# Kernel tuning notes

Hardware: AMD Instinct MI355X
Metric: run time of the kernel (lower is better)

## Reference

```python
import jax, jax.numpy as jnp
import numpy as np

TOP_K = 2
CAPACITY_FACTOR = 1.0


def _ffn(x, w1, w2):
    # SwiGLU FFN: x [N, D], w1 [D, 2F], w2 [F, D]
    h = x @ w1
    x1, x2 = jnp.split(h, 2, axis=-1)
    return (x1 * jax.nn.silu(x2)) @ w2


def setup_inputs() -> dict:
    key = jax.random.key(0)
    ks = jax.random.split(key, 6)
    B, S, D, F, E_r, E_s = 4, 2048, 2048, 1024, 7, 1
    sc_in = 1.0 / np.sqrt(D)
    sc_mid = 1.0 / np.sqrt(F)
    return {
        "x": jax.random.normal(ks[0], (B, S, D), dtype=jnp.float32),
        "gate_w": jax.random.normal(ks[1], (D, E_r), dtype=jnp.float32) * sc_in,
        "expert_bias": jnp.zeros((E_r,), dtype=jnp.float32),
        "shared_w1": jax.random.normal(ks[2], (E_s, D, 2 * F), dtype=jnp.float32) * sc_in,
        "shared_w2": jax.random.normal(ks[3], (E_s, F, D), dtype=jnp.float32) * sc_mid,
        "routed_w1": jax.random.normal(ks[4], (E_r, D, 2 * F), dtype=jnp.float32) * sc_in,
        "routed_w2": jax.random.normal(ks[5], (E_r, F, D), dtype=jnp.float32) * sc_mid,
    }


def reference(x, gate_w, expert_bias, shared_w1, shared_w2, routed_w1, routed_w2):
    B, S, D = x.shape
    E_r = gate_w.shape[1]
    T = B * S
    capacity = max(1, int(CAPACITY_FACTOR * T / E_r))
    flat_x = x.reshape(T, D)

    # shared experts: applied to every token, summed
    shared_sum = jax.vmap(_ffn, in_axes=(None, 0, 0))(flat_x, shared_w1, shared_w2).sum(0)

    # gating (eval mode: no noise, no dropout)
    gate_logits = flat_x @ gate_w + expert_bias  # [T, E_r]
    aff = jax.nn.sigmoid(gate_logits)
    _, topk_idx = jax.lax.top_k(aff, TOP_K)  # [T, K]
    # mask[t, e] = expert e is among token t's top-k
    mask = (topk_idx[:, :, None] == jnp.arange(E_r)[None, None, :]).any(axis=1)  # [T, E_r]

    # per-expert capacity selection: keep top-`capacity` masked tokens by affinity
    score = jnp.where(mask, aff, -1.0).T  # [E_r, T]; aff >= 0 so -1 sorts last
    _, sel_idx = jax.lax.top_k(score, capacity)  # [E_r, capacity] token ids
    kept = jnp.take_along_axis(mask.T, sel_idx, axis=1)  # [E_r, cap]
    w = jnp.where(kept, jnp.take_along_axis(aff.T, sel_idx, axis=1), 0.0)  # [E_r, cap]

    # grouped gather -> FFN -> weighted scatter-add
    inp = flat_x[sel_idx]  # [E_r, cap, D]
    out = jax.vmap(_ffn)(inp, routed_w1, routed_w2)  # [E_r, cap, D]
    routed_sum = jnp.zeros_like(flat_x).at[sel_idx].add(out * w[:, :, None])

    return (shared_sum + routed_sum).reshape(B, S, D)
```

## Files before the change

kernel.cpp:

```cpp
#include <hip/hip_runtime.h>
#include <hip/hip_bf16.h>

typedef unsigned long long u64;
typedef __bf16 bf16x8 __attribute__((ext_vector_type(8)));
typedef float f32x4 __attribute__((ext_vector_type(4)));
typedef unsigned short ushort8_t __attribute__((ext_vector_type(8)));

#define TOKS 8192
#define DMODEL 2048
#define FD 1024
#define NEXP 7
#define CAP 1170
#define CAPP 1280
#define URT 134

#define MFMA16(a, b, c) __builtin_amdgcn_mfma_f32_16x16x32_bf16(a, b, c, 0, 0, 0)

__device__ __forceinline__ unsigned short f2bf(float f) {
  __hip_bfloat16 b = __float2bfloat16(f);
  return __builtin_bit_cast(unsigned short, b);
}
__device__ __forceinline__ float bf2f(unsigned short u) {
  __hip_bfloat16 b = __builtin_bit_cast(__hip_bfloat16, u);
  return __bfloat162float(b);
}
__device__ __forceinline__ void gload_lds16(const void* g, void* l) {
  __builtin_amdgcn_global_load_lds(
      (const __attribute__((address_space(1))) void*)g,
      (__attribute__((address_space(3))) void*)l, 16, 0, 0);
}

__global__ __launch_bounds__(256) void k_conv_gate(
    const float* __restrict__ x, const float* __restrict__ gw,
    const float* __restrict__ bias, unsigned short* __restrict__ xb,
    u64* __restrict__ keys) {
  const int t = blockIdx.x;
  const int tid = threadIdx.x;
  const int lane = tid & 63, wv = tid >> 6;
  const float* xr = x + (long)t * DMODEL;
  const int i0 = tid * 8;
  float4 v0 = *(const float4*)&xr[i0];
  float4 v1 = *(const float4*)&xr[i0 + 4];
  float xv[8] = {v0.x, v0.y, v0.z, v0.w, v1.x, v1.y, v1.z, v1.w};
  ushort8_t o;
#pragma unroll
  for (int j = 0; j < 8; ++j) o[j] = f2bf(xv[j]);
  *(ushort8_t*)&xb[(long)t * DMODEL + i0] = o;
  double acc[NEXP];
#pragma unroll
  for (int e = 0; e < NEXP; ++e) acc[e] = 0.0;
#pragma unroll
  for (int j = 0; j < 8; ++j) {
    const float* g = gw + (long)(i0 + j) * NEXP;
    double xd = (double)xv[j];
#pragma unroll
    for (int e = 0; e < NEXP; ++e) acc[e] += xd * (double)g[e];
  }
#pragma unroll
  for (int e = 0; e < NEXP; ++e)
    for (int off = 32; off > 0; off >>= 1)
      acc[e] += __shfl_down(acc[e], off, 64);
  __shared__ double red[4][NEXP];
  if (lane == 0)
#pragma unroll
    for (int e = 0; e < NEXP; ++e) red[wv][e] = acc[e];
  __syncthreads();
  if (tid == 0) {
    float aff[NEXP];
#pragma unroll
    for (int e = 0; e < NEXP; ++e) {
      double lg = red[0][e] + red[1][e] + red[2][e] + red[3][e] + (double)bias[e];
      aff[e] = (float)(1.0 / (1.0 + exp(-lg)));
    }
    int i1 = 0;
    for (int e = 1; e < NEXP; ++e) if (aff[e] > aff[i1]) i1 = e;
    int i2 = -1;
    for (int e = 0; e < NEXP; ++e) {
      if (e == i1) continue;
      if (i2 < 0 || aff[e] > aff[i2]) i2 = e;
    }
#pragma unroll
    for (int e = 0; e < NEXP; ++e) {
      u64 key = (u64)(0xFFFFFFFFu - (unsigned)t);
      if (e == i1 || e == i2) key |= ((u64)__float_as_uint(aff[e])) << 32;
      keys[(long)e * TOKS + t] = key;
    }
  }
}

template <bool PERM>
__global__ void k_transpose_bf16(const float* __restrict__ in0,
                                 const float* __restrict__ inr,
                                 unsigned short* __restrict__ out,
                                 int R, int C) {
  __shared__ float tile[32][33];
  int z = blockIdx.z;
  const float* in = (z == 0) ? in0 : (inr + (long)(z - 1) * R * C);
  unsigned short* o = out + (long)z * R * C;
  int c0 = blockIdx.x * 32;
  int r0 = blockIdx.y * 32;
  int tx = threadIdx.x, ty = threadIdx.y;
#pragma unroll
  for (int k = 0; k < 4; ++k)
    tile[ty + 8 * k][tx] = in[(long)(r0 + ty + 8 * k) * C + c0 + tx];
  __syncthreads();
#pragma unroll
  for (int k = 0; k < 4; ++k) {
    int c = c0 + ty + 8 * k;
    long orow = PERM ? (long)(((c & 1023) >> 4) * 32 + ((c >> 10) << 4) + (c & 15))
                     : (long)c;
    o[orow * R + r0 + tx] = f2bf(tile[tx][ty + 8 * k]);
  }
}

__global__ __launch_bounds__(1024) void k_select(
    const u64* __restrict__ keys, int* __restrict__ sel,
    float* __restrict__ selw, unsigned* __restrict__ cnt,
    int* __restrict__ inv) {
  __shared__ unsigned hist[256];
  __shared__ u64 s_prefix;
  __shared__ unsigned s_k;
  __shared__ unsigned s_cnt;
  const int e = blockIdx.x;
  const u64* kk = keys + (long)e * TOKS;
  const int tid = threadIdx.x;
  if (tid == 0) { s_prefix = 0; s_k = CAP; s_cnt = 0; }
  __syncthreads();
  for (int shift = 56; shift >= 0; shift -= 8) {
    if (tid < 256) hist[tid] = 0;
    __syncthreads();
    u64 pref = s_prefix;
    for (int i = tid; i < TOKS; i += 1024) {
      u64 key = kk[i];
      bool match = (shift == 56) || ((key >> (shift + 8)) == pref);
      if (match) atomicAdd(&hist[(unsigned)(key >> shift) & 255u], 1u);
    }
    __syncthreads();
    if (tid == 0) {
      unsigned k = s_k, cum = 0;
      for (int b = 255; b >= 0; --b) {
        unsigned c = hist[b];
        if (cum + c >= k) {
          s_prefix = (s_prefix << 8) | (unsigned)b;
          s_k = k - cum;
          break;
        }
        cum += c;
      }
    }
    __syncthreads();
  }
  const u64 T = s_prefix;
  for (int i = tid; i < TOKS; i += 1024) {
    u64 key = kk[i];
    if (key >= T) {
      unsigned p = atomicAdd(&s_cnt, 1u);
      int tok = (int)(0xFFFFFFFFu - (unsigned)(key & 0xFFFFFFFFull));
      unsigned vb = (unsigned)(key >> 32);
      sel[e * CAPP + p] = tok;
      selw[e * CAPP + p] = vb ? __uint_as_float(vb) : 0.0f;
      if (vb) {
        unsigned pos = atomicAdd(&cnt[tok], 1u);
        inv[tok * 2 + pos] = e * CAPP + (int)p;
      }
    }
  }
  for (int i = CAP + tid; i < CAPP; i += 1024) {
    sel[e * CAPP + i] = 0;
    selw[e * CAPP + i] = 0.0f;
  }
}

__global__ __launch_bounds__(256) void k_combine(
    float* __restrict__ out, const unsigned short* __restrict__ rout,
    const int* __restrict__ inv, const unsigned* __restrict__ cnt) {
  const int tok = blockIdx.x;
  const unsigned c = cnt[tok];
  if (c == 0) return;
  int i0 = inv[tok * 2];
  int i1 = (c > 1) ? inv[tok * 2 + 1] : -1;
  if (c > 1 && i1 < i0) { int t = i0; i0 = i1; i1 = t; }
  const int col = threadIdx.x * 8;
  float* o = out + (long)tok * DMODEL + col;
  float4 v0 = *(float4*)o;
  float4 v1 = *(float4*)(o + 4);
  ushort8_t r0 = *(const ushort8_t*)&rout[(long)i0 * DMODEL + col];
  v0.x += bf2f(r0[0]); v0.y += bf2f(r0[1]); v0.z += bf2f(r0[2]); v0.w += bf2f(r0[3]);
  v1.x += bf2f(r0[4]); v1.y += bf2f(r0[5]); v1.z += bf2f(r0[6]); v1.w += bf2f(r0[7]);
  if (c > 1) {
    ushort8_t r1 = *(const ushort8_t*)&rout[(long)i1 * DMODEL + col];
    v0.x += bf2f(r1[0]); v0.y += bf2f(r1[1]); v0.z += bf2f(r1[2]); v0.w += bf2f(r1[3]);
    v1.x += bf2f(r1[4]); v1.y += bf2f(r1[5]); v1.z += bf2f(r1[6]); v1.w += bf2f(r1[7]);
  }
  *(float4*)o = v0;
  *(float4*)(o + 4) = v1;
}

template <int WHICH>
__global__ __launch_bounds__(256, 4) void k_ffn(
    const unsigned short* __restrict__ Abase,
    const unsigned short* __restrict__ Wbase,
    unsigned short* __restrict__ a_all, float* __restrict__ out,
    unsigned short* __restrict__ r_out,
    const int* __restrict__ sel, const float* __restrict__ selw) {
  constexpr int K = (WHICH == 1) ? DMODEL : FD;
  constexpr int N = (WHICH == 1) ? 2 * FD : DMODEL;
  constexpr int nk = K >> 5;
  __shared__ unsigned short lds[2][8192];
  const int tid = threadIdx.x;
  const int w = tid >> 6;
  const int lane = tid & 63;

  int lin = blockIdx.x + ((int)blockIdx.y << 4);
  int gt = (lin & 7) * 268 + (lin >> 3);
  int ct, rt;
  int su;
  if (gt < 2048) { su = gt >> 7; int rr = gt & 127; ct = rr >> 3; rt = rr & 7; }
  else           { su = 16;      int rr = gt - 2048; ct = rr / 6; rt = rr % 6; }
  const int by_u = su * 8 + rt;
  const int bx = ct;

  int e, zw, m0l;
  if (by_u < 64) { e = -1; zw = 0; m0l = by_u << 7; }
  else { int q = by_u - 64; e = q / 10; zw = e + 1; m0l = (q % 10) << 7; }
  const long crow0_u = (e < 0) ? (long)m0l : (8192 + (long)e * CAPP + m0l);
  const long n0 = (long)bx * 128;
  const unsigned short* Bm = Wbase + (long)zw * N * K;

  const int r_ = (w << 4) + (lane >> 2);
  const int p_ = lane & 3;
  const unsigned short* aSrc[2];
  const unsigned short* bSrc[2];
#pragma unroll
  for (int c = 0; c < 2; ++c) {
    int rsg = c * 64 + r_;
    int q = p_ ^ ((rsg >> 1) & 3);
    long arow;
    if (WHICH == 1)
      arow = (e < 0) ? (long)(m0l + rsg) : (long)sel[e * CAPP + m0l + rsg];
    else
      arow = crow0_u + rsg;
    aSrc[c] = Abase + arow * (long)K + q * 8;
    bSrc[c] = Bm + (n0 + rsg) * (long)K + q * 8;
  }
  const int dst0 = tid * 8;

  auto STAGE = [&](int buf, int kt) {
    const long ko = (long)kt * 32;
#pragma unroll
    for (int c = 0; c < 2; ++c) {
      gload_lds16(aSrc[c] + ko, &lds[buf][c * 2048 + dst0]);
      gload_lds16(bSrc[c] + ko, &lds[buf][4096 + c * 2048 + dst0]);
    }
  };

  const int wr = w >> 1, wc = w & 1;
  const int lr = lane & 15, kq = lane >> 4;
  const int slot = (kq ^ ((lr >> 1) & 3)) * 8;
  const int aRow = wr * 64 + lr;
  const int bRow = wc * 64 + lr;

  STAGE(0, 0);
  asm volatile("s_waitcnt vmcnt(0)" ::: "memory");
  __builtin_amdgcn_sched_barrier(0);
  __builtin_amdgcn_s_barrier();
  __builtin_amdgcn_sched_barrier(0);

  f32x4 acc[4][4] = {};
  int cur = 0;

#pragma unroll 1
  for (int kt = 0; kt < nk; ++kt) {
    if (kt + 1 < nk) STAGE(cur ^ 1, kt + 1);
    const unsigned short* aSeg = &lds[cur][0];
    const unsigned short* bSeg = &lds[cur][4096];
    bf16x8 af[4], bf[4];
#pragma unroll
    for (int m = 0; m < 4; ++m)
      af[m] = *(const bf16x8*)&aSeg[(aRow + m * 16) * 32 + slot];
#pragma unroll
    for (int n = 0; n < 4; ++n)
      bf[n] = *(const bf16x8*)&bSeg[(bRow + n * 16) * 32 + slot];
    asm volatile("s_waitcnt lgkmcnt(0)" ::: "memory");
    __builtin_amdgcn_sched_barrier(0);
    __builtin_amdgcn_s_setprio(1);
#pragma unroll
    for (int m = 0; m < 4; ++m)
#pragma unroll
      for (int n = 0; n < 4; ++n)
        acc[m][n] = MFMA16(af[m], bf[n], acc[m][n]);
    __builtin_amdgcn_s_setprio(0);
    asm volatile("s_waitcnt vmcnt(0)" ::: "memory");
    __builtin_amdgcn_sched_barrier(0);
    __builtin_amdgcn_s_barrier();
    __builtin_amdgcn_sched_barrier(0);
    cur ^= 1;
  }

  const int r0q = (lane >> 4) * 4;
  const int cc = lane & 15;

  if (WHICH == 1) {
    const long gcol0 = (n0 >> 1) + wc * 32;
#pragma unroll
    for (int m = 0; m < 4; ++m)
#pragma unroll
      for (int rj = 0; rj < 4; ++rj) {
        long row = crow0_u + wr * 64 + m * 16 + r0q + rj;
#pragma unroll
        for (int q2 = 0; q2 < 2; ++q2) {
          float x1v = acc[m][2 * q2][rj];
          float x2v = acc[m][2 * q2 + 1][rj];
          float s = x2v / (1.0f + __expf(-x2v));
          a_all[row * FD + gcol0 + q2 * 16 + cc] = f2bf(x1v * s);
        }
      }
  } else {
    const long ccol0 = n0 + wc * 64;
    if (e < 0) {
#pragma unroll
      for (int m = 0; m < 4; ++m)
#pragma unroll
        for (int rj = 0; rj < 4; ++rj) {
          long row = m0l + wr * 64 + m * 16 + r0q + rj;
#pragma unroll
          for (int n = 0; n < 4; ++n)
            out[row * DMODEL + ccol0 + n * 16 + cc] = acc[m][n][rj];
        }
    } else {
#pragma unroll
      for (int m = 0; m < 4; ++m)
#pragma unroll
        for (int rj = 0; rj < 4; ++rj) {
          int lrow = m0l + wr * 64 + m * 16 + r0q + rj;
          float wgt = selw[e * CAPP + lrow];
          unsigned short* C = r_out + ((long)e * CAPP + lrow) * DMODEL;
#pragma unroll
          for (int n = 0; n < 4; ++n)
            C[ccol0 + n * 16 + cc] = f2bf(acc[m][n][rj] * wgt);
        }
    }
  }
}

extern "C" void kernel_launch(void* const* d_in, const int* in_sizes, int n_in,
                              void* d_out, int out_size, void* d_ws,
                              size_t ws_size, hipStream_t stream) {
  (void)in_sizes; (void)n_in; (void)out_size; (void)ws_size;
  const float* x = (const float*)d_in[0];
  const float* gw = (const float*)d_in[1];
  const float* eb = (const float*)d_in[2];
  const float* sw1 = (const float*)d_in[3];
  const float* sw2 = (const float*)d_in[4];
  const float* rw1 = (const float*)d_in[5];
  const float* rw2 = (const float*)d_in[6];
  float* out = (float*)d_out;

  char* ws = (char*)d_ws;
  size_t off = 0;
  auto alloc = [&](size_t bytes) {
    size_t o = off;
    off += (bytes + 255) & ~(size_t)255;
    return o;
  };
  unsigned short* xb    = (unsigned short*)(ws + alloc((size_t)TOKS * DMODEL * 2));
  unsigned short* w1t   = (unsigned short*)(ws + alloc((size_t)8 * DMODEL * (2 * FD) * 2));
  unsigned short* w2t   = (unsigned short*)(ws + alloc((size_t)8 * DMODEL * FD * 2));
  unsigned short* a_all = (unsigned short*)(ws + alloc((size_t)(TOKS + NEXP * CAPP) * FD * 2));
  unsigned short* r_out = (unsigned short*)(ws + alloc((size_t)NEXP * CAPP * DMODEL * 2));
  u64* keys = (u64*)(ws + alloc((size_t)NEXP * TOKS * 8));
  int* sel  = (int*)(ws + alloc((size_t)NEXP * CAPP * 4));
  float* selw = (float*)(ws + alloc((size_t)NEXP * CAPP * 4));
  unsigned* cnt = (unsigned*)(ws + alloc((size_t)TOKS * 4));
  int* inv = (int*)(ws + alloc((size_t)TOKS * 2 * 4));

  k_conv_gate<<<TOKS, 256, 0, stream>>>(x, gw, eb, xb, keys);
  dim3 tb(32, 8);
  k_transpose_bf16<true><<<dim3(64, 64, 8), tb, 0, stream>>>(sw1, rw1, w1t, DMODEL, 2 * FD);
  k_transpose_bf16<false><<<dim3(64, 32, 8), tb, 0, stream>>>(sw2, rw2, w2t, FD, DMODEL);
  hipMemsetAsync(cnt, 0, (size_t)TOKS * 4, stream);
  k_select<<<NEXP, 1024, 0, stream>>>(keys, sel, selw, cnt, inv);
  k_ffn<1><<<dim3(16, URT), 256, 0, stream>>>(xb, w1t, a_all, nullptr, nullptr,
                                              sel, nullptr);
  k_ffn<2><<<dim3(16, URT), 256, 0, stream>>>(a_all, w2t, nullptr, out, r_out,
                                              nullptr, selw);
  k_combine<<<TOKS, 256, 0, stream>>>(out, r_out, inv, cnt);
}
```

Before: 495.8 us.

## Widen weight transpose tiles, fold memset into gate, unify FFN2 bf16 output

Replaces the 32x32 weight transpose with a 64x64 tile kernel that uses float4 loads and 16-byte bf16 stores. Zeroes the per-token counters inside the gate kernel so the separate memset goes away. FFN2 now writes both shared and routed results as bf16 into one buffer, and the combine kernel writes the final fp32 output once instead of reading and modifying it. The FFN kernels switch to dynamic LDS, with launch bounds lowered to 3 waves and a larger LDS allocation that reduces occupancy. Storing the shared-expert output as bf16 adds rounding error.

```diff
diff --git a/kernel.cpp b/kernel.cpp
--- a/kernel.cpp
+++ b/kernel.cpp
@@ -12,7 +12,7 @@
 #define NEXP 7
 #define CAP 1170
 #define CAPP 1280
-#define URT 134
+#define URT128 134
 
 #define MFMA16(a, b, c) __builtin_amdgcn_mfma_f32_16x16x32_bf16(a, b, c, 0, 0, 0)
 
@@ -33,10 +33,11 @@
 __global__ __launch_bounds__(256) void k_conv_gate(
     const float* __restrict__ x, const float* __restrict__ gw,
     const float* __restrict__ bias, unsigned short* __restrict__ xb,
-    u64* __restrict__ keys) {
+    u64* __restrict__ keys, unsigned* __restrict__ cnt) {
   const int t = blockIdx.x;
   const int tid = threadIdx.x;
   const int lane = tid & 63, wv = tid >> 6;
+  if (tid == 0) cnt[t] = 0;
   const float* xr = x + (long)t * DMODEL;
   const int i0 = tid * 8;
   float4 v0 = *(const float4*)&xr[i0];
@@ -89,27 +90,40 @@
 }
 
 template <bool PERM>
-__global__ void k_transpose_bf16(const float* __restrict__ in0,
-                                 const float* __restrict__ inr,
-                                 unsigned short* __restrict__ out,
-                                 int R, int C) {
-  __shared__ float tile[32][33];
-  int z = blockIdx.z;
+__global__ __launch_bounds__(256) void k_tr64(
+    const float* __restrict__ in0, const float* __restrict__ inr,
+    unsigned short* __restrict__ out, int R, int C) {
+  __shared__ float t[64][65];
+  const int z = blockIdx.z;
   const float* in = (z == 0) ? in0 : (inr + (long)(z - 1) * R * C);
   unsigned short* o = out + (long)z * R * C;
-  int c0 = blockIdx.x * 32;
-  int r0 = blockIdx.y * 32;
-  int tx = threadIdx.x, ty = threadIdx.y;
-#pragma unroll
-  for (int k = 0; k < 4; ++k)
-    tile[ty + 8 * k][tx] = in[(long)(r0 + ty + 8 * k) * C + c0 + tx];
+  const int c0 = blockIdx.x * 64;
+  const int r0 = blockIdx.y * 64;
+  const int tid = threadIdx.x;
+  const int rr = tid >> 4;
+  const int cc4 = (tid & 15) * 4;
+#pragma unroll
+  for (int i = 0; i < 4; ++i) {
+    int r = rr + 16 * i;
+    float4 v = *(const float4*)&in[(long)(r0 + r) * C + c0 + cc4];
+    t[r][cc4 + 0] = v.x;
+    t[r][cc4 + 1] = v.y;
+    t[r][cc4 + 2] = v.z;
+    t[r][cc4 + 3] = v.w;
+  }
   __syncthreads();
 #pragma unroll
-  for (int k = 0; k < 4; ++k) {
-    int c = c0 + ty + 8 * k;
-    long orow = PERM ? (long)(((c & 1023) >> 4) * 32 + ((c >> 10) << 4) + (c & 15))
-                     : (long)c;
-    o[orow * R + r0 + tx] = f2bf(tile[tx][ty + 8 * k]);
+  for (int h = 0; h < 2; ++h) {
+    int c = tid + h * 256;
+    int oc = c >> 3;
+    int j = c & 7;
+    ushort8_t v8;
+#pragma unroll
+    for (int q = 0; q < 8; ++q) v8[q] = f2bf(t[j * 8 + q][oc]);
+    int gc = c0 + oc;
+    long orow = PERM ? (long)(((gc & 1023) >> 4) * 32 + ((gc >> 10) << 4) + (gc & 15))
+                     : (long)gc;
+    *(ushort8_t*)&o[orow * R + r0 + j * 8] = v8;
   }
 }
 
@@ -172,49 +186,55 @@
 }
 
 __global__ __launch_bounds__(256) void k_combine(
-    float* __restrict__ out, const unsigned short* __restrict__ rout,
+    float* __restrict__ out, const unsigned short* __restrict__ o_all,
     const int* __restrict__ inv, const unsigned* __restrict__ cnt) {
   const int tok = blockIdx.x;
   const unsigned c = cnt[tok];
-  if (c == 0) return;
-  int i0 = inv[tok * 2];
-  int i1 = (c > 1) ? inv[tok * 2 + 1] : -1;
-  if (c > 1 && i1 < i0) { int t = i0; i0 = i1; i1 = t; }
+  int i0 = -1, i1 = -1;
+  if (c > 0) {
+    i0 = inv[tok * 2];
+    if (c > 1) {
+      i1 = inv[tok * 2 + 1];
+      if (i1 < i0) { int t = i0; i0 = i1; i1 = t; }
+    }
+  }
   const int col = threadIdx.x * 8;
-  float* o = out + (long)tok * DMODEL + col;
-  float4 v0 = *(float4*)o;
-  float4 v1 = *(float4*)(o + 4);
-  ushort8_t r0 = *(const ushort8_t*)&rout[(long)i0 * DMODEL + col];
-  v0.x += bf2f(r0[0]); v0.y += bf2f(r0[1]); v0.z += bf2f(r0[2]); v0.w += bf2f(r0[3]);
-  v1.x += bf2f(r0[4]); v1.y += bf2f(r0[5]); v1.z += bf2f(r0[6]); v1.w += bf2f(r0[7]);
-  if (c > 1) {
-    ushort8_t r1 = *(const ushort8_t*)&rout[(long)i1 * DMODEL + col];
-    v0.x += bf2f(r1[0]); v0.y += bf2f(r1[1]); v0.z += bf2f(r1[2]); v0.w += bf2f(r1[3]);
-    v1.x += bf2f(r1[4]); v1.y += bf2f(r1[5]); v1.z += bf2f(r1[6]); v1.w += bf2f(r1[7]);
-  }
-  *(float4*)o = v0;
-  *(float4*)(o + 4) = v1;
+  ushort8_t s = *(const ushort8_t*)&o_all[(long)tok * DMODEL + col];
+  float v[8];
+#pragma unroll
+  for (int q = 0; q < 8; ++q) v[q] = bf2f(s[q]);
+  if (i0 >= 0) {
+    ushort8_t r = *(const ushort8_t*)&o_all[(long)(TOKS + i0) * DMODEL + col];
+#pragma unroll
+    for (int q = 0; q < 8; ++q) v[q] += bf2f(r[q]);
+  }
+  if (i1 >= 0) {
+    ushort8_t r = *(const ushort8_t*)&o_all[(long)(TOKS + i1) * DMODEL + col];
+#pragma unroll
+    for (int q = 0; q < 8; ++q) v[q] += bf2f(r[q]);
+  }
+  float* op = out + (long)tok * DMODEL + col;
+  *(float4*)op = make_float4(v[0], v[1], v[2], v[3]);
+  *(float4*)(op + 4) = make_float4(v[4], v[5], v[6], v[7]);
 }
 
 template <int WHICH>
-__global__ __launch_bounds__(256, 4) void k_ffn(
+__global__ __launch_bounds__(256, 3) void k_ffn(
     const unsigned short* __restrict__ Abase,
     const unsigned short* __restrict__ Wbase,
-    unsigned short* __restrict__ a_all, float* __restrict__ out,
-    unsigned short* __restrict__ r_out,
-    const int* __restrict__ sel, const float* __restrict__ selw) {
+    unsigned short* __restrict__ obuf, const int* __restrict__ sel,
+    const float* __restrict__ selw) {
   constexpr int K = (WHICH == 1) ? DMODEL : FD;
-  constexpr int N = (WHICH == 1) ? 2 * FD : DMODEL;
+  constexpr int N = 2048;
   constexpr int nk = K >> 5;
-  __shared__ unsigned short lds[2][8192];
+  extern __shared__ unsigned short lds[];
   const int tid = threadIdx.x;
   const int w = tid >> 6;
   const int lane = tid & 63;
 
   int lin = blockIdx.x + ((int)blockIdx.y << 4);
   int gt = (lin & 7) * 268 + (lin >> 3);
-  int ct, rt;
-  int su;
+  int ct, rt, su;
   if (gt < 2048) { su = gt >> 7; int rr = gt & 127; ct = rr >> 3; rt = rr & 7; }
   else           { su = 16;      int rr = gt - 2048; ct = rr / 6; rt = rr % 6; }
   const int by_u = su * 8 + rt;
@@ -246,11 +266,12 @@
   const int dst0 = tid * 8;
 
   auto STAGE = [&](int buf, int kt) {
+    unsigned short* bufp = lds + buf * 8192;
     const long ko = (long)kt * 32;
 #pragma unroll
     for (int c = 0; c < 2; ++c) {
-      gload_lds16(aSrc[c] + ko, &lds[buf][c * 2048 + dst0]);
-      gload_lds16(bSrc[c] + ko, &lds[buf][4096 + c * 2048 + dst0]);
+      gload_lds16(aSrc[c] + ko, bufp + c * 2048 + dst0);
+      gload_lds16(bSrc[c] + ko, bufp + 4096 + c * 2048 + dst0);
     }
   };
 
@@ -272,8 +293,8 @@
 #pragma unroll 1
   for (int kt = 0; kt < nk; ++kt) {
     if (kt + 1 < nk) STAGE(cur ^ 1, kt + 1);
-    const unsigned short* aSeg = &lds[cur][0];
-    const unsigned short* bSeg = &lds[cur][4096];
+    const unsigned short* aSeg = lds + cur * 8192;
+    const unsigned short* bSeg = aSeg + 4096;
     bf16x8 af[4], bf[4];
 #pragma unroll
     for (int m = 0; m < 4; ++m)
@@ -312,34 +333,22 @@
           float x1v = acc[m][2 * q2][rj];
           float x2v = acc[m][2 * q2 + 1][rj];
           float s = x2v / (1.0f + __expf(-x2v));
-          a_all[row * FD + gcol0 + q2 * 16 + cc] = f2bf(x1v * s);
+          obuf[row * FD + gcol0 + q2 * 16 + cc] = f2bf(x1v * s);
         }
       }
   } else {
     const long ccol0 = n0 + wc * 64;
-    if (e < 0) {
-#pragma unroll
-      for (int m = 0; m < 4; ++m)
-#pragma unroll
-        for (int rj = 0; rj < 4; ++rj) {
-          long row = m0l + wr * 64 + m * 16 + r0q + rj;
-#pragma unroll
-          for (int n = 0; n < 4; ++n)
-            out[row * DMODEL + ccol0 + n * 16 + cc] = acc[m][n][rj];
-        }
-    } else {
-#pragma unroll
-      for (int m = 0; m < 4; ++m)
-#pragma unroll
-        for (int rj = 0; rj < 4; ++rj) {
-          int lrow = m0l + wr * 64 + m * 16 + r0q + rj;
-          float wgt = selw[e * CAPP + lrow];
-          unsigned short* C = r_out + ((long)e * CAPP + lrow) * DMODEL;
-#pragma unroll
-          for (int n = 0; n < 4; ++n)
-            C[ccol0 + n * 16 + cc] = f2bf(acc[m][n][rj] * wgt);
-        }
-    }
+#pragma unroll
+    for (int m = 0; m < 4; ++m)
+#pragma unroll
+      for (int rj = 0; rj < 4; ++rj) {
+        int lrow = m0l + wr * 64 + m * 16 + r0q + rj;
+        float wgt = (e < 0) ? 1.0f : selw[e * CAPP + lrow];
+        long row = crow0_u + wr * 64 + m * 16 + r0q + rj;
+#pragma unroll
+        for (int n = 0; n < 4; ++n)
+          obuf[row * DMODEL + ccol0 + n * 16 + cc] = f2bf(acc[m][n][rj] * wgt);
+      }
   }
 }
 
@@ -367,22 +376,20 @@
   unsigned short* w1t   = (unsigned short*)(ws + alloc((size_t)8 * DMODEL * (2 * FD) * 2));
   unsigned short* w2t   = (unsigned short*)(ws + alloc((size_t)8 * DMODEL * FD * 2));
   unsigned short* a_all = (unsigned short*)(ws + alloc((size_t)(TOKS + NEXP * CAPP) * FD * 2));
-  unsigned short* r_out = (unsigned short*)(ws + alloc((size_t)NEXP * CAPP * DMODEL * 2));
+  unsigned short* o_all = (unsigned short*)(ws + alloc((size_t)(TOKS + NEXP * CAPP) * DMODEL * 2));
   u64* keys = (u64*)(ws + alloc((size_t)NEXP * TOKS * 8));
   int* sel  = (int*)(ws + alloc((size_t)NEXP * CAPP * 4));
   float* selw = (float*)(ws + alloc((size_t)NEXP * CAPP * 4));
   unsigned* cnt = (unsigned*)(ws + alloc((size_t)TOKS * 4));
   int* inv = (int*)(ws + alloc((size_t)TOKS * 2 * 4));
 
-  k_conv_gate<<<TOKS, 256, 0, stream>>>(x, gw, eb, xb, keys);
-  dim3 tb(32, 8);
-  k_transpose_bf16<true><<<dim3(64, 64, 8), tb, 0, stream>>>(sw1, rw1, w1t, DMODEL, 2 * FD);
-  k_transpose_bf16<false><<<dim3(64, 32, 8), tb, 0, stream>>>(sw2, rw2, w2t, FD, DMODEL);
-  hipMemsetAsync(cnt, 0, (size_t)TOKS * 4, stream);
+  const size_t LDS3 = 54272;
+
+  k_conv_gate<<<TOKS, 256, 0, stream>>>(x, gw, eb, xb, keys, cnt);
+  k_tr64<true><<<dim3(32, 32, 8), 256, 0, stream>>>(sw1, rw1, w1t, DMODEL, 2 * FD);
+  k_tr64<false><<<dim3(32, 16, 8), 256, 0, stream>>>(sw2, rw2, w2t, FD, DMODEL);
   k_select<<<NEXP, 1024, 0, stream>>>(keys, sel, selw, cnt, inv);
-  k_ffn<1><<<dim3(16, URT), 256, 0, stream>>>(xb, w1t, a_all, nullptr, nullptr,
-                                              sel, nullptr);
-  k_ffn<2><<<dim3(16, URT), 256, 0, stream>>>(a_all, w2t, nullptr, out, r_out,
-                                              nullptr, selw);
-  k_combine<<<TOKS, 256, 0, stream>>>(out, r_out, inv, cnt);
-}
+  k_ffn<1><<<dim3(16, URT128), 256, LDS3, stream>>>(xb, w1t, a_all, sel, nullptr);
+  k_ffn<2><<<dim3(16, URT128), 256, LDS3, stream>>>(a_all, w2t, o_all, nullptr, selw);
+  k_combine<<<TOKS, 256, 0, stream>>>(out, o_all, inv, cnt);
+}
```

After: 544.3 us. +9.8%, slower.
